# Optimization experiments

Measured on AMD Instinct MI355X. Metric: run time of the kernel, lower is better.

## Reference

```python
import jax, jax.numpy as jnp
import numpy as np

D, M, B, K = 512, 128, 16, 4
COHERENCE_COEFF = 0.01
LAMBDA_COEFF = 1.0


def setup_inputs() -> dict:
    key = jax.random.key(0)
    k1, k2, k3, k4 = jax.random.split(key, 4)
    x = jax.random.normal(k1, (2, 2048, D), dtype=jnp.float32)
    V = jax.random.normal(k2, (D, M, B), dtype=jnp.float32)
    U = jax.random.normal(k3, (M, D, B), dtype=jnp.float32)
    u_scales = jax.random.normal(k4, (M, B), dtype=jnp.float32)
    return {"x": x, "V": V, "U": U, "u_scales": u_scales}


def _forward(x, V, U, u_scales):
    # UnitColNorm parametrizations: normalize over the D axis
    Vn = V / jnp.linalg.norm(V, axis=0, keepdims=True)          # (D, m, b)
    Un = U / jnp.linalg.norm(U, axis=1, keepdims=True)          # (m, D, b)
    s = jnp.tanh(u_scales) * LAMBDA_COEFF                        # (m, b)
    U_eff = Un * s[:, None, :]                                   # (m, D, b)

    expert_reprs = jnp.einsum('...d,dmb->...mb', x, Vn)          # (..., m, b)
    repr_l2_sq = jnp.sum(expert_reprs * expert_reprs, axis=-1)   # (..., m)
    topk_vals, topk_idxs = jax.lax.top_k(repr_l2_sq, K)          # (..., k)

    reprs_topk = jnp.take_along_axis(expert_reprs, topk_idxs[..., None], axis=-2)  # (..., k, b)
    U_active = U_eff[topk_idxs]                                  # (..., k, D, b)
    writes = jnp.einsum('...kdb,...kb->...d', U_active, reprs_topk)

    # aux terms
    N = topk_vals.size // K
    idxs_flat = topk_idxs.reshape(-1)
    vals_flat = topk_vals.reshape(-1)
    energy_per_expert = jnp.zeros((M,), dtype=vals_flat.dtype).at[idxs_flat].add(vals_flat) / N
    select_rate = jnp.zeros((M,), dtype=vals_flat.dtype).at[idxs_flat].add(1.0) / N
    total_energy = jnp.maximum(energy_per_expert.sum(), 1e-12)
    relative_energy = energy_per_expert / total_energy

    eye = jnp.eye(M * B, dtype=Vn.dtype)
    sqrtD = jnp.sqrt(jnp.asarray(D, dtype=Vn.dtype))

    def coherence_penalty(Mtx):
        G = Mtx.T @ Mtx  # (m*b, m*b)
        return jnp.abs(G - eye).mean() * sqrtD

    v_pen = coherence_penalty(Vn.reshape(D, M * B))
    u_pen = coherence_penalty(U_eff.transpose(1, 0, 2).reshape(D, M * B))
    aux_loss = COHERENCE_COEFF * v_pen - total_energy

    out = x + writes
    return (out, total_energy, energy_per_expert, relative_energy,
            select_rate, v_pen, u_pen, aux_loss)


def reference(x, V, U, u_scales):
    return _forward(x, V, U, u_scales)
```

## Files before the change

### kernel.cpp

```cpp
#include <hip/hip_runtime.h>
#include <math.h>

#define D 512
#define M 128
#define B 16
#define KSEL 4
#define NC 2048
#define NTOK 4096

typedef unsigned short ushort;
typedef unsigned int uint;
typedef unsigned long long u64;
typedef __attribute__((ext_vector_type(8))) short short8;
typedef __attribute__((ext_vector_type(4))) float floatx4;

#define WS_EACC   0
#define WS_CACC   128
#define WS_VSUM   256
#define WS_USUM   257
#define WS_CNT_I  258
#define WS_VSCALE 512
#define WS_USCALE 2560
#define WS_E_F    4608
#define WS_RBF_F  528896
#define WS_XH_F   2626048
#define WS_XL_F   3674624
#define WS_VHT_F  4723200
#define WS_VLT_F  5247488
#define WS_UHT_F  5771776
#define WS_ULT_F  6296064
#define WS_LIST_F 6820352
#define WS_SEL_F  7344640

#define OUT_TE   2097152
#define OUT_EPE  2097153
#define OUT_RE   2097281
#define OUT_SR   2097409
#define OUT_VPEN 2097537
#define OUT_UPEN 2097538
#define OUT_AUX  2097539

#define GLDS16(g, l) __builtin_amdgcn_global_load_lds(                        \
    (const __attribute__((address_space(1))) unsigned int*)(g),               \
    (__attribute__((address_space(3))) unsigned int*)(l), 16, 0, 0)

__device__ __forceinline__ ushort f2bf(float f) {
    union { float f; uint u; } a; a.f = f;
    uint u = a.u;
    u += 0x7fffu + ((u >> 16) & 1u);
    return (ushort)(u >> 16);
}
__device__ __forceinline__ float bf2f(ushort h) {
    union { uint u; float f; } a; a.u = ((uint)h) << 16;
    return a.f;
}

__launch_bounds__(256)
__global__ void prep_kernel(const float* __restrict__ x, const float* __restrict__ V,
                            const float* __restrict__ U, const float* __restrict__ us_in,
                            ushort* __restrict__ xh, ushort* __restrict__ xl,
                            ushort* __restrict__ vht, ushort* __restrict__ vlt,
                            ushort* __restrict__ uht, ushort* __restrict__ ult,
                            float* __restrict__ ws) {
    __shared__ float ts[64][65];
    const int bid = blockIdx.x;
    const int tid = threadIdx.x;

    if (bid < 1024) {
        const int idx = (bid * 256 + tid) * 8;
        float4 v0 = *(const float4*)(x + idx);
        float4 v1 = *(const float4*)(x + idx + 4);
        float vv[8] = {v0.x, v0.y, v0.z, v0.w, v1.x, v1.y, v1.z, v1.w};
        union { ushort u[8]; uint4 q; } H, L;
#pragma unroll
        for (int j = 0; j < 8; ++j) {
            ushort h = f2bf(vv[j]);
            H.u[j] = h;
            L.u[j] = f2bf(vv[j] - bf2f(h));
        }
        *(uint4*)(xh + idx) = H.q;
        *(uint4*)(xl + idx) = L.q;
    } else if (bid < 1280) {
        const int vb = bid - 1024;
        const int col0 = (vb & 31) * 64;
        const int d0 = (vb >> 5) * 64;
#pragma unroll
        for (int i = 0; i < 16; ++i) {
            int idx = i * 256 + tid;
            int r = idx >> 6, c = idx & 63;
            ts[r][c] = V[(size_t)(d0 + r) * NC + col0 + c];
        }
        __syncthreads();
#pragma unroll
        for (int i = 0; i < 16; ++i) {
            int idx = i * 256 + tid;
            int c2 = idx >> 6, d2 = idx & 63;
            float v = ts[d2][c2];
            ushort h = f2bf(v);
            vht[(size_t)(col0 + c2) * D + d0 + d2] = h;
            vlt[(size_t)(col0 + c2) * D + d0 + d2] = f2bf(v - bf2f(h));
        }
    } else if (bid < 1408) {
        const int m = bid - 1280;
        float (*t2)[129] = (float (*)[129])ts;
        for (int d0 = 0; d0 < D; d0 += 128) {
            __syncthreads();
#pragma unroll
            for (int i = 0; i < 8; ++i) {
                int idx = i * 256 + tid;
                int d2 = idx >> 4, b2 = idx & 15;
                t2[b2][d2] = U[(size_t)m * (D * B) + (size_t)(d0 + d2) * B + b2];
            }
            __syncthreads();
#pragma unroll
            for (int i = 0; i < 8; ++i) {
                int idx = i * 256 + tid;
                int b3 = idx >> 7, d3 = idx & 127;
                float v = t2[b3][d3];
                ushort h = f2bf(v);
                uht[(size_t)((m << 4) + b3) * D + d0 + d3] = h;
                ult[(size_t)((m << 4) + b3) * D + d0 + d3] = f2bf(v - bf2f(h));
            }
        }
    } else {
        const int bx = bid - 1408;
        if (bx >= 160) {
            ws[(bx - 160) * 256 + tid] = 0.0f;
            return;
        }
        if (bx < 32) {
            const int c = bx * 64 + (tid & 63);
            const int dg = tid >> 6;
            float s = 0.0f;
            for (int d = dg; d < D; d += 4) {
                float v = V[(size_t)d * NC + c];
                s = fmaf(v, v, s);
            }
            float (*sh)[64] = (float (*)[64])ts;
            sh[dg][tid & 63] = s;
            __syncthreads();
            if (tid < 64) {
                float t = (sh[0][tid] + sh[1][tid]) + (sh[2][tid] + sh[3][tid]);
                ws[WS_VSCALE + bx * 64 + tid] = 1.0f / sqrtf(t);
            }
        } else {
            const int m = bx - 32;
            const float* p = U + (size_t)m * (D * B);
            float s = 0.0f;
            for (int i = tid; i < D * B; i += 256) {
                float v = p[i];
                s = fmaf(v, v, s);
            }
            float* sh2 = &ts[0][0];
            sh2[tid] = s;
            __syncthreads();
            if (tid < 16) {
                float t = 0.0f;
#pragma unroll
                for (int j = 0; j < 16; ++j) t += sh2[tid + (j << 4)];
                ws[WS_USCALE + (m << 4) + tid] = tanhf(us_in[(m << 4) + tid]) / sqrtf(t);
            }
        }
    }
}

__launch_bounds__(256)
__global__ void mfma_fused(const ushort* __restrict__ xh, const ushort* __restrict__ xl,
                           const ushort* __restrict__ vht, const ushort* __restrict__ vlt,
                           const ushort* __restrict__ uht, const ushort* __restrict__ ult,
                           float* __restrict__ ws, ushort* __restrict__ rbf) {
    __shared__ ushort smem[16384];
    const int bid = blockIdx.x;
    const int tid = threadIdx.x, lane = tid & 63, w = tid >> 6;
    const int wr = w >> 1, wc = w & 1;
    const int r15 = lane & 15, q = lane >> 4;
    const int srl = lane >> 2;
    const int skq = (lane & 3) ^ ((lane >> 3) & 3);
    const int perm8 = (q ^ ((r15 >> 1) & 3)) * 8;

    const int is_gemm = bid < 512;
    const ushort* srcs[4];
    int rbase[4];
    int gi = 0, gj = 0, which = 0;
    if (is_gemm) {
        const int x = bid & 7, inner = bid >> 3;
        const int tokG = ((x >> 1) << 3) + (inner & 7);
        const int colG = ((x & 1) << 3) + (inner >> 3);
        const int tokB = tokG * 128, colB = colG * 128;
        srcs[0] = xh; srcs[1] = xl; srcs[2] = vht; srcs[3] = vlt;
        rbase[0] = tokB; rbase[1] = tokB; rbase[2] = colB; rbase[3] = colB;
    } else {
        int t = bid - 512;
        which = t >= 136;
        if (which) t -= 136;
        int bi = 0, rem = 16;
        while (t >= rem) { t -= rem; --rem; ++bi; }
        gi = bi; gj = bi + t;
        const ushort* ht = which ? uht : vht;
        srcs[0] = ht; srcs[1] = ht; srcs[2] = ht; srcs[3] = ht;
        rbase[0] = gi * 128; rbase[1] = gi * 128; rbase[2] = gj * 128; rbase[3] = gj * 128;
    }

    floatx4 acc[4][4];
#pragma unroll
    for (int i = 0; i < 4; ++i)
#pragma unroll
        for (int j = 0; j < 4; ++j) acc[i][j] = (floatx4){0.f, 0.f, 0.f, 0.f};

    auto stage = [&](int c) {
        const int kb = c * 32 + skq * 8;
#pragma unroll
        for (int tI = 0; tI < 4; ++tI) {
            if (!is_gemm && (tI & 1)) continue;
            const ushort* s = srcs[tI] + (size_t)rbase[tI] * D + kb;
#pragma unroll
            for (int sub = 0; sub < 2; ++sub) {
                const int row16 = w * 32 + sub * 16;
                GLDS16(s + (size_t)(row16 + srl) * D,
                       &smem[tI * 4096 + row16 * 32]);
            }
        }
    };

    stage(0);
    for (int c = 0; c < 16; ++c) {
        __syncthreads();
        short8 ah[4], al[4], bh[4], bl[4];
#pragma unroll
        for (int s = 0; s < 4; ++s) {
            const int ra = (wr * 64 + s * 16 + r15) * 32 + perm8;
            ah[s] = *(const short8*)&smem[ra];
            const int rb = (wc * 64 + s * 16 + r15) * 32 + perm8;
            bh[s] = *(const short8*)&smem[8192 + rb];
            if (is_gemm) {
                al[s] = *(const short8*)&smem[4096 + ra];
                bl[s] = *(const short8*)&smem[12288 + rb];
            }
        }
        __syncthreads();
        if (c < 15) stage(c + 1);
#pragma unroll
        for (int st = 0; st < 4; ++st)
#pragma unroll
            for (int sc = 0; sc < 4; ++sc) {
                acc[st][sc] = __builtin_amdgcn_mfma_f32_16x16x32_bf16(ah[st], bh[sc], acc[st][sc], 0, 0, 0);
                if (is_gemm) {
                    acc[st][sc] = __builtin_amdgcn_mfma_f32_16x16x32_bf16(ah[st], bl[sc], acc[st][sc], 0, 0, 0);
                    acc[st][sc] = __builtin_amdgcn_mfma_f32_16x16x32_bf16(al[st], bh[sc], acc[st][sc], 0, 0, 0);
                }
            }
    }

    if (is_gemm) {
        const int tok0 = rbase[0] + wr * 64, col0 = rbase[2] + wc * 64;
        const int cg4 = col0 >> 6;
        float* e2base = ws + WS_E_F + (size_t)cg4 * (NTOK * 4);
#pragma unroll
        for (int st = 0; st < 4; ++st) {
            const int rowb = tok0 + st * 16 + q * 4;
            float er[4][4];
#pragma unroll
            for (int sc = 0; sc < 4; ++sc) {
                const int colg = col0 + sc * 16 + r15;
                const float vs = ws[WS_VSCALE + colg];
                float r0 = acc[st][sc][0] * vs;
                float r1 = acc[st][sc][1] * vs;
                float r2 = acc[st][sc][2] * vs;
                float r3 = acc[st][sc][3] * vs;
                rbf[(size_t)(rowb + 0) * NC + colg] = f2bf(r0);
                rbf[(size_t)(rowb + 1) * NC + colg] = f2bf(r1);
                rbf[(size_t)(rowb + 2) * NC + colg] = f2bf(r2);
                rbf[(size_t)(rowb + 3) * NC + colg] = f2bf(r3);
                float e0 = r0 * r0, e1 = r1 * r1, e2 = r2 * r2, e3 = r3 * r3;
#pragma unroll
                for (int mk = 1; mk < 16; mk <<= 1) {
                    e0 += __shfl_xor(e0, mk);
                    e1 += __shfl_xor(e1, mk);
                    e2 += __shfl_xor(e2, mk);
                    e3 += __shfl_xor(e3, mk);
                }
                er[sc][0] = e0; er[sc][1] = e1; er[sc][2] = e2; er[sc][3] = e3;
            }
            if (r15 == 0) {
#pragma unroll
                for (int j = 0; j < 4; ++j) {
                    *(float4*)(e2base + (size_t)(rowb + j) * 4) =
                        make_float4(er[0][j], er[1][j], er[2][j], er[3][j]);
                }
            }
        }
    } else {
        const float* scl = ws + (which ? WS_USCALE : WS_VSCALE);
        float* sum_out = ws + (which ? WS_USUM : WS_VSUM);
        float local = 0.0f;
#pragma unroll
        for (int sc = 0; sc < 4; ++sc) {
            const int colg = gj * 128 + wc * 64 + sc * 16 + r15;
            const float scj = scl[colg];
#pragma unroll
            for (int st = 0; st < 4; ++st) {
#pragma unroll
                for (int reg = 0; reg < 4; ++reg) {
                    const int rowg = gi * 128 + wr * 64 + st * 16 + q * 4 + reg;
                    float g = acc[st][sc][reg] * scl[rowg] * scj;
                    if (rowg == colg) g -= 1.0f;
                    local += fabsf(g);
                }
            }
        }
        if (gi < gj) local *= 2.0f;
#pragma unroll
        for (int mk = 1; mk < 64; mk <<= 1) local += __shfl_xor(local, mk);
        __shared__ float red[4];
        if (lane == 0) red[w] = local;
        __syncthreads();
        if (tid == 0) atomicAdd(sum_out, (red[0] + red[1]) + (red[2] + red[3]));
    }
}

__launch_bounds__(256)
__global__ void topk_kernel(float* __restrict__ ws) {
    const int tid = threadIdx.x, lane = tid & 63, w = tid >> 6;
    const int t = blockIdx.x * 4 + w;

    const int cg4 = lane >> 1;
    const int e2off = (lane & 1) * 2;
    const float2 ev = *(const float2*)(ws + WS_E_F +
                                       ((size_t)cg4 * NTOK + t) * 4 + e2off);
    const uint i0 = (uint)(lane * 2), i1 = i0 + 1;
    u64 k0 = ((u64)__float_as_uint(ev.x) << 32) | (uint)(~i0);
    u64 k1 = ((u64)__float_as_uint(ev.y) << 32) | (uint)(~i1);
    u64 s0 = k0 > k1 ? k0 : k1;
    u64 s1 = k0 > k1 ? k1 : k0;
    u64 s2 = 0, s3 = 0;

#pragma unroll
    for (int mk = 1; mk < 64; mk <<= 1) {
        u64 o0 = __shfl_xor(s0, mk);
        u64 o1 = __shfl_xor(s1, mk);
        u64 o2 = __shfl_xor(s2, mk);
        u64 o3 = __shfl_xor(s3, mk);
        u64 c0 = s0 > o3 ? s0 : o3;
        u64 c1 = s1 > o2 ? s1 : o2;
        u64 c2 = s2 > o1 ? s2 : o1;
        u64 c3 = s3 > o0 ? s3 : o0;
        u64 d0 = c0 > c2 ? c0 : c2, d2 = c0 > c2 ? c2 : c0;
        u64 d1 = c1 > c3 ? c1 : c3, d3 = c1 > c3 ? c3 : c1;
        s0 = d0 > d1 ? d0 : d1; s1 = d0 > d1 ? d1 : d0;
        s2 = d2 > d3 ? d2 : d3; s3 = d2 > d3 ? d3 : d2;
    }

    if (lane < 4) {
        u64 key = (lane == 0) ? s0 : (lane == 1) ? s1 : (lane == 2) ? s2 : s3;
        const uint e = (uint)(~(uint)key) & 127u;
        const u64 lo = ((u64)(e << 14)) | (u64)((t << 2) | lane);
        ((u64*)(ws + WS_SEL_F))[(t << 2) + lane] =
            (key & 0xFFFFFFFF00000000ull) | lo;
    }
}

__launch_bounds__(256)
__global__ void listbuild_kernel(float* __restrict__ ws) {
    const int e = blockIdx.x;
    const int tid = threadIdx.x;
    const u64* sels = (const u64*)(ws + WS_SEL_F);
    int* icnt = (int*)ws + WS_CNT_I;
    int* ilist = (int*)(ws + WS_LIST_F) + (e << 12);

    __shared__ int sc_[256];
    __shared__ float sv[256];

    const int base_idx = tid * 64;
    int cnt = 0;
    float vsum = 0.0f;
#pragma unroll 8
    for (int j = 0; j < 64; ++j) {
        u64 s = sels[base_idx + j];
        if ((int)((s >> 14) & 127u) == e) {
            ++cnt;
            vsum += __uint_as_float((uint)(s >> 32));
        }
    }
    sc_[tid] = cnt;
    sv[tid] = vsum;
    __syncthreads();

#pragma unroll
    for (int off = 1; off < 256; off <<= 1) {
        int v = (tid >= off) ? sc_[tid - off] : 0;
        __syncthreads();
        sc_[tid] += v;
        __syncthreads();
    }
    const int wbase = sc_[tid] - cnt;
    const int total = sc_[255];

    if (cnt > 0) {
        int p = wbase;
#pragma unroll 8
        for (int j = 0; j < 64; ++j) {
            u64 s = sels[base_idx + j];
            if ((int)((s >> 14) & 127u) == e)
                ilist[p++] = (int)(s & 0x3FFFu);
        }
    }

#pragma unroll
    for (int off = 128; off > 0; off >>= 1) {
        __syncthreads();
        if (tid < off) sv[tid] += sv[tid + off];
    }
    if (tid == 0) {
        icnt[e] = total;
        ws[WS_EACC + e] = sv[0];
        ws[WS_CACC + e] = (float)total;
    }
}

__launch_bounds__(256)
__global__ void expert_contrib_kernel(const float* __restrict__ U,
                                      const ushort* __restrict__ rbf,
                                      const float* __restrict__ ws,
                                      uint* __restrict__ contrib) {
    const int e = blockIdx.x;
    const int tid = threadIdx.x;
    const int cnt = ((const int*)ws)[WS_CNT_I + e];
    if ((int)blockIdx.y >= cnt) return;

    float usc[16];
#pragma unroll
    for (int b = 0; b < 16; ++b) usc[b] = ws[WS_USCALE + (e << 4) + b];

    const float* Up = U + (size_t)e * (D * B);
    float u0[16], u1[16];
#pragma unroll
    for (int qd = 0; qd < 4; ++qd) {
        float4 a = *(const float4*)(Up + (size_t)(2 * tid) * B + qd * 4);
        float4 b4 = *(const float4*)(Up + (size_t)(2 * tid + 1) * B + qd * 4);
        u0[qd * 4 + 0] = a.x * usc[qd * 4 + 0];
        u0[qd * 4 + 1] = a.y * usc[qd * 4 + 1];
        u0[qd * 4 + 2] = a.z * usc[qd * 4 + 2];
        u0[qd * 4 + 3] = a.w * usc[qd * 4 + 3];
        u1[qd * 4 + 0] = b4.x * usc[qd * 4 + 0];
        u1[qd * 4 + 1] = b4.y * usc[qd * 4 + 1];
        u1[qd * 4 + 2] = b4.z * usc[qd * 4 + 2];
        u1[qd * 4 + 3] = b4.w * usc[qd * 4 + 3];
    }

    const int* ilist = (const int*)(ws + WS_LIST_F) + (e << 12);
    int i = blockIdx.y;
    int pk = (i < cnt) ? ilist[i] : 0;
    while (i < cnt) {
        const int t = pk >> 2, k = pk & 3;
        const ushort* rp = rbf + (size_t)t * NC + (e << 4);
        union { ushort u[16]; uint4 q[2]; } R;
        R.q[0] = *(const uint4*)(rp);
        R.q[1] = *(const uint4*)(rp + 8);
        const int inext = i + 4;
        if (inext < cnt) pk = ilist[inext];
        float acc0 = 0.0f, acc1 = 0.0f;
#pragma unroll
        for (int b = 0; b < 16; ++b) {
            const float wv = bf2f(R.u[b]);
            acc0 = fmaf(u0[b], wv, acc0);
            acc1 = fmaf(u1[b], wv, acc1);
        }
        contrib[(size_t)((t << 2) + k) * 256 + tid] =
            (uint)f2bf(acc0) | ((uint)f2bf(acc1) << 16);
        i = inext;
    }
}

__launch_bounds__(256)
__global__ void combine_kernel(const float* __restrict__ x,
                               const uint* __restrict__ contrib,
                               const float* __restrict__ ws,
                               float* __restrict__ out) {
    if (blockIdx.x == 1024) {
        const int m = threadIdx.x;
        if (m >= 128) return;
        float e = ws[WS_EACC + m] * (1.0f / (float)NTOK);
        float c = ws[WS_CACC + m] * (1.0f / (float)NTOK);
        float s = e;
#pragma unroll
        for (int off = 32; off > 0; off >>= 1) s += __shfl_down(s, off);
        __shared__ float sh[2];
        if ((m & 63) == 0) sh[m >> 6] = s;
        __syncthreads();
        float total = sh[0] + sh[1];
        float total_energy = fmaxf(total, 1e-12f);
        out[OUT_EPE + m] = e;
        out[OUT_RE + m] = e / total_energy;
        out[OUT_SR + m] = c;
        if (m == 0) {
            out[OUT_TE] = total_energy;
            float inv_n2 = 1.0f / ((float)NC * (float)NC);
            float sqrtD = sqrtf((float)D);
            float vpen = ws[WS_VSUM] * inv_n2 * sqrtD;
            float upen = ws[WS_USUM] * inv_n2 * sqrtD;
            out[OUT_VPEN] = vpen;
            out[OUT_UPEN] = upen;
            out[OUT_AUX] = 0.01f * vpen - total_energy;
        }
        return;
    }

    const int gid = blockIdx.x * 256 + threadIdx.x;
    const int t = gid >> 6;
    const int dq = (gid & 63) << 3;
    const uint4* cp = (const uint4*)contrib;

    float s[8];
    float4 x0 = *(const float4*)(x + (size_t)t * D + dq);
    float4 x1 = *(const float4*)(x + (size_t)t * D + dq + 4);
    s[0] = x0.x; s[1] = x0.y; s[2] = x0.z; s[3] = x0.w;
    s[4] = x1.x; s[5] = x1.y; s[6] = x1.z; s[7] = x1.w;
#pragma unroll
    for (int k = 0; k < KSEL; ++k) {
        uint4 cvec = cp[(size_t)((t << 2) + k) * 64 + (dq >> 3)];
        uint cc[4] = {cvec.x, cvec.y, cvec.z, cvec.w};
#pragma unroll
        for (int j = 0; j < 4; ++j) {
            s[2 * j]     += bf2f((ushort)(cc[j] & 0xffffu));
            s[2 * j + 1] += bf2f((ushort)(cc[j] >> 16));
        }
    }
    float* op = out + (size_t)t * D + dq;
    *(float4*)(op)     = make_float4(s[0], s[1], s[2], s[3]);
    *(float4*)(op + 4) = make_float4(s[4], s[5], s[6], s[7]);
}

extern "C" void kernel_launch(void* const* d_in, const int* in_sizes, int n_in,
                              void* d_out, int out_size, void* d_ws, size_t ws_size,
                              hipStream_t stream) {
    const float* x  = (const float*)d_in[0];
    const float* V  = (const float*)d_in[1];
    const float* U  = (const float*)d_in[2];
    const float* us = (const float*)d_in[3];
    float* out = (float*)d_out;
    float* ws  = (float*)d_ws;

    ushort* xh  = (ushort*)(ws + WS_XH_F);
    ushort* xl  = (ushort*)(ws + WS_XL_F);
    ushort* vht = (ushort*)(ws + WS_VHT_F);
    ushort* vlt = (ushort*)(ws + WS_VLT_F);
    ushort* uht = (ushort*)(ws + WS_UHT_F);
    ushort* ult = (ushort*)(ws + WS_ULT_F);
    ushort* rbf = (ushort*)(ws + WS_RBF_F);
    uint* contrib = (uint*)(ws + WS_XH_F);

    prep_kernel<<<1570, 256, 0, stream>>>(x, V, U, us, xh, xl, vht, vlt, uht, ult, ws);
    mfma_fused<<<784, 256, 0, stream>>>(xh, xl, vht, vlt, uht, ult, ws, rbf);
    topk_kernel<<<NTOK / 4, 256, 0, stream>>>(ws);
    listbuild_kernel<<<M, 256, 0, stream>>>(ws);
    expert_contrib_kernel<<<dim3(128, 4), 256, 0, stream>>>(U, rbf, ws, contrib);
    combine_kernel<<<1025, 256, 0, stream>>>(x, contrib, ws, out);
}
```

Baseline: 168.4 us.

## Split gram path to direct-load MFMA, drop unused U low part, widen expert grid

The Gram-matrix blocks of the fused MFMA kernel get their own loop that loads bf16 fragments straight from global memory into registers, with no LDS staging and no block barriers. The GEMM path keeps its LDS pipeline but no longer carries per-iteration is_gemm branches. The prep kernel stops writing the unused low-bf16 half of U. The expert contribution kernel launches twice as many y-blocks, each striding by 8, to raise parallelism. The risk is that uncoalesced direct global loads in the Gram path expose more memory latency.

```diff
diff --git a/kernel.cpp b/kernel.cpp
--- a/kernel.cpp
+++ b/kernel.cpp
@@ -116,10 +116,7 @@
             for (int i = 0; i < 8; ++i) {
                 int idx = i * 256 + tid;
                 int b3 = idx >> 7, d3 = idx & 127;
-                float v = t2[b3][d3];
-                ushort h = f2bf(v);
-                uht[(size_t)((m << 4) + b3) * D + d0 + d3] = h;
-                ult[(size_t)((m << 4) + b3) * D + d0 + d3] = f2bf(v - bf2f(h));
+                uht[(size_t)((m << 4) + b3) * D + d0 + d3] = f2bf(t2[b3][d3]);
             }
         }
     } else {
@@ -179,80 +176,61 @@
     const int perm8 = (q ^ ((r15 >> 1) & 3)) * 8;
 
     const int is_gemm = bid < 512;
-    const ushort* srcs[4];
-    int rbase[4];
-    int gi = 0, gj = 0, which = 0;
+
+    floatx4 acc[4][4];
+#pragma unroll
+    for (int i = 0; i < 4; ++i)
+#pragma unroll
+        for (int j = 0; j < 4; ++j) acc[i][j] = (floatx4){0.f, 0.f, 0.f, 0.f};
+
     if (is_gemm) {
-        const int x = bid & 7, inner = bid >> 3;
-        const int tokG = ((x >> 1) << 3) + (inner & 7);
-        const int colG = ((x & 1) << 3) + (inner >> 3);
+        const int xs = bid & 7, inner = bid >> 3;
+        const int tokG = ((xs >> 1) << 3) + (inner & 7);
+        const int colG = ((xs & 1) << 3) + (inner >> 3);
         const int tokB = tokG * 128, colB = colG * 128;
-        srcs[0] = xh; srcs[1] = xl; srcs[2] = vht; srcs[3] = vlt;
-        rbase[0] = tokB; rbase[1] = tokB; rbase[2] = colB; rbase[3] = colB;
-    } else {
-        int t = bid - 512;
-        which = t >= 136;
-        if (which) t -= 136;
-        int bi = 0, rem = 16;
-        while (t >= rem) { t -= rem; --rem; ++bi; }
-        gi = bi; gj = bi + t;
-        const ushort* ht = which ? uht : vht;
-        srcs[0] = ht; srcs[1] = ht; srcs[2] = ht; srcs[3] = ht;
-        rbase[0] = gi * 128; rbase[1] = gi * 128; rbase[2] = gj * 128; rbase[3] = gj * 128;
-    }
-
-    floatx4 acc[4][4];
-#pragma unroll
-    for (int i = 0; i < 4; ++i)
-#pragma unroll
-        for (int j = 0; j < 4; ++j) acc[i][j] = (floatx4){0.f, 0.f, 0.f, 0.f};
-
-    auto stage = [&](int c) {
-        const int kb = c * 32 + skq * 8;
-#pragma unroll
-        for (int tI = 0; tI < 4; ++tI) {
-            if (!is_gemm && (tI & 1)) continue;
-            const ushort* s = srcs[tI] + (size_t)rbase[tI] * D + kb;
-#pragma unroll
-            for (int sub = 0; sub < 2; ++sub) {
-                const int row16 = w * 32 + sub * 16;
-                GLDS16(s + (size_t)(row16 + srl) * D,
-                       &smem[tI * 4096 + row16 * 32]);
-            }
-        }
-    };
-
-    stage(0);
-    for (int c = 0; c < 16; ++c) {
-        __syncthreads();
-        short8 ah[4], al[4], bh[4], bl[4];
-#pragma unroll
-        for (int s = 0; s < 4; ++s) {
-            const int ra = (wr * 64 + s * 16 + r15) * 32 + perm8;
-            ah[s] = *(const short8*)&smem[ra];
-            const int rb = (wc * 64 + s * 16 + r15) * 32 + perm8;
-            bh[s] = *(const short8*)&smem[8192 + rb];
-            if (is_gemm) {
+        const ushort* srcs[4] = {xh, xl, vht, vlt};
+        const int rbase[4] = {tokB, tokB, colB, colB};
+
+        auto stage = [&](int c) {
+            const int kb = c * 32 + skq * 8;
+#pragma unroll
+            for (int tI = 0; tI < 4; ++tI) {
+                const ushort* s = srcs[tI] + (size_t)rbase[tI] * D + kb;
+#pragma unroll
+                for (int sub = 0; sub < 2; ++sub) {
+                    const int row16 = w * 32 + sub * 16;
+                    GLDS16(s + (size_t)(row16 + srl) * D,
+                           &smem[tI * 4096 + row16 * 32]);
+                }
+            }
+        };
+
+        stage(0);
+        for (int c = 0; c < 16; ++c) {
+            __syncthreads();
+            short8 ah[4], al[4], bh[4], bl[4];
+#pragma unroll
+            for (int s = 0; s < 4; ++s) {
+                const int ra = (wr * 64 + s * 16 + r15) * 32 + perm8;
+                ah[s] = *(const short8*)&smem[ra];
                 al[s] = *(const short8*)&smem[4096 + ra];
+                const int rb = (wc * 64 + s * 16 + r15) * 32 + perm8;
+                bh[s] = *(const short8*)&smem[8192 + rb];
                 bl[s] = *(const short8*)&smem[12288 + rb];
             }
-        }
-        __syncthreads();
-        if (c < 15) stage(c + 1);
-#pragma unroll
-        for (int st = 0; st < 4; ++st)
-#pragma unroll
-            for (int sc = 0; sc < 4; ++sc) {
-                acc[st][sc] = __builtin_amdgcn_mfma_f32_16x16x32_bf16(ah[st], bh[sc], acc[st][sc], 0, 0, 0);
-                if (is_gemm) {
+            __syncthreads();
+            if (c < 15) stage(c + 1);
+#pragma unroll
+            for (int st = 0; st < 4; ++st)
+#pragma unroll
+                for (int sc = 0; sc < 4; ++sc) {
+                    acc[st][sc] = __builtin_amdgcn_mfma_f32_16x16x32_bf16(ah[st], bh[sc], acc[st][sc], 0, 0, 0);
                     acc[st][sc] = __builtin_amdgcn_mfma_f32_16x16x32_bf16(ah[st], bl[sc], acc[st][sc], 0, 0, 0);
                     acc[st][sc] = __builtin_amdgcn_mfma_f32_16x16x32_bf16(al[st], bh[sc], acc[st][sc], 0, 0, 0);
                 }
-            }
-    }
-
-    if (is_gemm) {
-        const int tok0 = rbase[0] + wr * 64, col0 = rbase[2] + wc * 64;
+        }
+
+        const int tok0 = tokB + wr * 64, col0 = colB + wc * 64;
         const int cg4 = col0 >> 6;
         float* e2base = ws + WS_E_F + (size_t)cg4 * (NTOK * 4);
 #pragma unroll
@@ -290,6 +268,33 @@
             }
         }
     } else {
+        int t = bid - 512;
+        const int which = t >= 136;
+        if (which) t -= 136;
+        int bi = 0, rem = 16;
+        while (t >= rem) { t -= rem; --rem; ++bi; }
+        const int gi = bi, gj = bi + t;
+        const ushort* ht = which ? uht : vht;
+        const int arow = gi * 128, brow = gj * 128;
+
+        const ushort* ap = ht + (size_t)(arow + wr * 64 + r15) * D + q * 8;
+        const ushort* bp = ht + (size_t)(brow + wc * 64 + r15) * D + q * 8;
+
+#pragma unroll 4
+        for (int c = 0; c < 16; ++c) {
+            short8 a[4], b[4];
+#pragma unroll
+            for (int s = 0; s < 4; ++s) {
+                a[s] = *(const short8*)(ap + (size_t)(s * 16) * D + c * 32);
+                b[s] = *(const short8*)(bp + (size_t)(s * 16) * D + c * 32);
+            }
+#pragma unroll
+            for (int st = 0; st < 4; ++st)
+#pragma unroll
+                for (int sc = 0; sc < 4; ++sc)
+                    acc[st][sc] = __builtin_amdgcn_mfma_f32_16x16x32_bf16(a[st], b[sc], acc[st][sc], 0, 0, 0);
+        }
+
         const float* scl = ws + (which ? WS_USCALE : WS_VSCALE);
         float* sum_out = ws + (which ? WS_USUM : WS_VSUM);
         float local = 0.0f;
@@ -456,7 +461,7 @@
         union { ushort u[16]; uint4 q[2]; } R;
         R.q[0] = *(const uint4*)(rp);
         R.q[1] = *(const uint4*)(rp + 8);
-        const int inext = i + 4;
+        const int inext = i + 8;
         if (inext < cnt) pk = ilist[inext];
         float acc0 = 0.0f, acc1 = 0.0f;
 #pragma unroll
@@ -553,6 +558,6 @@
     mfma_fused<<<784, 256, 0, stream>>>(xh, xl, vht, vlt, uht, ult, ws, rbf);
     topk_kernel<<<NTOK / 4, 256, 0, stream>>>(ws);
     listbuild_kernel<<<M, 256, 0, stream>>>(ws);
-    expert_contrib_kernel<<<dim3(128, 4), 256, 0, stream>>>(U, rbf, ws, contrib);
+    expert_contrib_kernel<<<dim3(128, 8), 256, 0, stream>>>(U, rbf, ws, contrib);
     combine_kernel<<<1025, 256, 0, stream>>>(x, contrib, ws, out);
 }
```

Result: slower. 184.7 us (+9.7%).
